# Optimization experiments

Hardware: AMD Instinct MI355X
Metric: run time of the kernel (lower is better)

## Reference

```python
import jax, jax.numpy as jnp
import numpy as np

N_NODES = 32000   # total nodes
NUM_GRAPHS = 32   # B
NODES_PER_GRAPH = 1000
N_EDGES = 256000
IN_DIM = 1024
HIDDEN = 256
C = 8             # clusters per graph


def sage_conv(x, src, dst, W_l, b_l, W_r, num_nodes):
    """PyG SAGEConv (mean aggr): out = lin_l(mean_{j in N(i)} x_j) + lin_r(x_i).
    lin_l has bias, lin_r does not. Zero in-degree -> zero aggregation."""
    msg = x[src]  # [E, F] gather from source nodes
    summed = jax.ops.segment_sum(msg, dst, num_segments=num_nodes)          # [N, F]
    cnt = jax.ops.segment_sum(jnp.ones(src.shape, x.dtype), dst, num_segments=num_nodes)  # [N]
    agg = jnp.where(cnt[:, None] > 0, summed / jnp.maximum(cnt, 1.0)[:, None], 0.0)
    return agg @ W_l + b_l + x @ W_r


def setup_inputs() -> dict:
    key = jax.random.key(0)
    ks = jax.random.split(key, 20)
    x = jax.random.normal(ks[0], (N_NODES, IN_DIM), dtype=jnp.float32)
    # edges strictly within each graph (nodes per graph contiguous)
    ge = jax.random.randint(ks[1], (N_EDGES,), 0, NUM_GRAPHS)
    sl = jax.random.randint(ks[2], (N_EDGES,), 0, NODES_PER_GRAPH)
    dl = jax.random.randint(ks[3], (N_EDGES,), 0, NODES_PER_GRAPH)
    edge_index = jnp.stack([ge * NODES_PER_GRAPH + sl, ge * NODES_PER_GRAPH + dl], axis=0)
    batch = jnp.arange(N_NODES, dtype=jnp.int32) // NODES_PER_GRAPH

    def lin(k, fi, fo):
        return jax.random.normal(k, (fi, fo), dtype=jnp.float32) / np.sqrt(fi)

    return {
        "x": x, "edge_index": edge_index, "batch": batch,
        # gnn_embed: SAGEConv(in_dim, hidden)
        "Wl1": lin(ks[4], IN_DIM, HIDDEN), "bl1": jnp.zeros((HIDDEN,), jnp.float32), "Wr1": lin(ks[5], IN_DIM, HIDDEN),
        # gnn_assign: SAGEConv(in_dim, C)
        "Wla": lin(ks[6], IN_DIM, C), "bla": jnp.zeros((C,), jnp.float32), "Wra": lin(ks[7], IN_DIM, C),
        # gnn_embed2: SAGEConv(hidden, hidden)
        "Wl2": lin(ks[8], HIDDEN, HIDDEN), "bl2": jnp.zeros((HIDDEN,), jnp.float32), "Wr2": lin(ks[9], HIDDEN, HIDDEN),
        # classifier MLP
        "Wc1": lin(ks[10], HIDDEN * C, HIDDEN), "bc1": jnp.zeros((HIDDEN,), jnp.float32),
        "Wc2": lin(ks[11], HIDDEN, 1), "bc2": jnp.zeros((1,), jnp.float32),
    }


def reference(x, edge_index, batch, Wl1, bl1, Wr1, Wla, bla, Wra, Wl2, bl2, Wr2, Wc1, bc1, Wc2, bc2):
    src, dst = edge_index[0], edge_index[1]
    n = x.shape[0]
    Z = jax.nn.relu(sage_conv(x, src, dst, Wl1, bl1, Wr1, n))   # [N, H]
    S = sage_conv(x, src, dst, Wla, bla, Wra, n)                 # [N, C]
    Ss = jax.nn.softmax(S, axis=-1)                              # row-softmax assignment
    # Per-graph DiffPool, batched via segment sums (replaces the python loop):
    # X_pool[g] = S_g^T Z_g
    Xp = jax.ops.segment_sum(Ss[:, :, None] * Z[:, None, :], batch, num_segments=NUM_GRAPHS)  # [B,C,H]
    # A_pool[g] = S_g^T A_g S_g  (A binary from to_dense_adj of within-graph edges)
    eg = batch[src]  # graph id per edge
    Ap = jax.ops.segment_sum(Ss[src][:, :, None] * Ss[dst][:, None, :], eg, num_segments=NUM_GRAPHS)  # [B,C,C]
    # dense_to_sparse(block_diag(A_pool)) drops edge weights -> binary block-diag adjacency.
    mask = (Ap != 0).astype(Z.dtype)   # edge i->j where A_pool[g,i,j] != 0
    deg = mask.sum(axis=1)             # in-degree of pooled node j: [B,C]
    agg = jnp.einsum('gij,gih->gjh', mask, Xp)  # mean over source pooled nodes
    agg = jnp.where(deg[:, :, None] > 0, agg / jnp.maximum(deg, 1.0)[:, :, None], 0.0)
    Zp = jax.nn.relu(agg @ Wl2 + bl2 + Xp @ Wr2)  # [B,C,H]
    g = Zp.reshape(NUM_GRAPHS, C * HIDDEN)
    h = jax.nn.relu(g @ Wc1 + bc1)
    return (h @ Wc2 + bc2).squeeze(-1)            # [B]
```

## Files before the change

kernel.cpp:

```cpp
#include <hip/hip_runtime.h>
#include <hip/hip_bf16.h>
#include <math.h>

#define N_NODES 32000
#define NUM_GRAPHS 32
#define NPG 1000
#define N_EDGES 256000
#define IN_DIM 1024
#define HID 256
#define NW 528
#define KBH 1040
#define WS_KS 33792
#define ZWORDS 139776

typedef _Float16 half8 __attribute__((ext_vector_type(8)));
typedef _Float16 half4 __attribute__((ext_vector_type(4)));
typedef float f32x4 __attribute__((ext_vector_type(4)));

__device__ __forceinline__ void gload16(const void* g, void* l) {
  __builtin_amdgcn_global_load_lds((const __attribute__((address_space(1))) void*)g,
                                   (__attribute__((address_space(3))) void*)l, 16, 0, 0);
}

__global__ __launch_bounds__(256) void prep_kernel(
    const float* __restrict__ Wl1, const float* __restrict__ Wr1,
    const float* __restrict__ Wla, const float* __restrict__ Wra,
    _Float16* __restrict__ WsT2, unsigned* __restrict__ zbuf)
{
  const int t = threadIdx.x;
  const int flat = blockIdx.y * 3 + blockIdx.x;
  for (int i = flat * 256 + t; i < ZWORDS; i += 384 * 256) zbuf[i] = 0u;

  const int kslot = blockIdx.y;
  const int n = blockIdx.x * 256 + t;
  if (n >= NW) return;
  const int k0 = kslot * 8;
  half8 o;
#pragma unroll
  for (int i = 0; i < 8; ++i) {
    const int k = k0 + i;
    float v;
    if (n < 256)      v = Wl1[(size_t)k * 256 + n];
    else if (n < 512) v = Wr1[(size_t)k * 256 + n - 256];
    else if (n < 520) v = Wla[(size_t)k * 8 + n - 512];
    else              v = Wra[(size_t)k * 8 + n - 520];
    o[i] = (_Float16)v;
  }
  const int ks = kslot >> 3, kb = kslot & 7;
  size_t off;
  if (n < 512) off = (size_t)ks * WS_KS + (size_t)(n >> 7) * 8192 + (kb * 128 + (n & 127)) * 8;
  else         off = (size_t)ks * WS_KS + 32768 + (kb * 16 + (n - 512)) * 8;
  *(half8*)&WsT2[off] = o;
}

__global__ __launch_bounds__(256) void xhalf(
    const float* __restrict__ x, _Float16* __restrict__ XH)
{
  const size_t i = ((size_t)blockIdx.x * 256 + threadIdx.x) * 8;
  float4 a = *(const float4*)(x + i);
  float4 b = *(const float4*)(x + i + 4);
  half8 h;
  h[0] = (_Float16)a.x; h[1] = (_Float16)a.y; h[2] = (_Float16)a.z; h[3] = (_Float16)a.w;
  h[4] = (_Float16)b.x; h[5] = (_Float16)b.y; h[6] = (_Float16)b.z; h[7] = (_Float16)b.w;
  *(half8*)&XH[i] = h;
}

__global__ __launch_bounds__(256) void gemm_mfma(
    const _Float16* __restrict__ XH, const _Float16* __restrict__ WsT2,
    _Float16* __restrict__ C)
{
  const int orig = blockIdx.x;
  const int xcd = orig & 7, idx = orig >> 3;
  const int g = (xcd < 2 ? xcd * 157 : 314 + (xcd - 2) * 156) + idx;
  const int pm = g / 5, nb = g % 5;
  const int m0 = pm * 128;

  __shared__ _Float16 AH[8 * KBH];
  __shared__ _Float16 Bs[8 * KBH];

  const int tid = threadIdx.x;
  const int w = tid >> 6, l = tid & 63;
  const int wr = w >> 1, wc = w & 1;
  const int r16 = l & 15, kb4 = l >> 4;

  int lpA[4];
  const _Float16* gA[4];
#pragma unroll
  for (int j = 0; j < 4; ++j) {
    const int c = tid + j * 256;
    const int kb = c >> 7, row = c & 127;
    lpA[j] = kb * KBH + row * 8;
    gA[j] = XH + (size_t)(m0 + row) * IN_DIM + kb * 8;
  }

  if (nb < 4) {
    const _Float16* gBbase = WsT2 + nb * 8192;

    f32x4 acc[4][4] = {};
    for (int ks = 0; ks < 16; ++ks) {
      const size_t ko = (size_t)ks * 64;
      const size_t bo = (size_t)ks * WS_KS;
      __syncthreads();
#pragma unroll
      for (int j = 0; j < 4; ++j) {
        gload16(gA[j] + ko, &AH[lpA[j]]);
        gload16(gBbase + bo + (tid + j * 256) * 8, &Bs[lpA[j]]);
      }
      __syncthreads();

#pragma unroll
      for (int s = 0; s < 2; ++s) {
        const int kblk = (s * 4 + kb4) * KBH;
        half8 bf[4];
#pragma unroll
        for (int n = 0; n < 4; ++n)
          bf[n] = *(half8*)&Bs[kblk + (wc * 64 + n * 16 + r16) * 8];
#pragma unroll
        for (int m = 0; m < 4; ++m) {
          half8 ah = *(half8*)&AH[kblk + (wr * 64 + m * 16 + r16) * 8];
#pragma unroll
          for (int n = 0; n < 4; ++n)
            acc[m][n] = __builtin_amdgcn_mfma_f32_16x16x32_f16(ah, bf[n], acc[m][n], 0, 0, 0);
        }
      }
    }
    const int crow0 = m0 + wr * 64 + ((l >> 4) << 2);
    const int ccol0 = nb * 128 + wc * 64 + r16;
#pragma unroll
    for (int m = 0; m < 4; ++m)
#pragma unroll
      for (int n = 0; n < 4; ++n)
#pragma unroll
        for (int r = 0; r < 4; ++r)
          C[(size_t)(crow0 + m * 16 + r) * NW + ccol0 + n * 16] = (_Float16)acc[m][n][r];
  } else {
    f32x4 acc2[2] = {};
    for (int ks = 0; ks < 16; ++ks) {
      const size_t ko = (size_t)ks * 64;
      const size_t bo = (size_t)ks * WS_KS + 32768;
      __syncthreads();
#pragma unroll
      for (int j = 0; j < 4; ++j) gload16(gA[j] + ko, &AH[lpA[j]]);
      if (tid < 128) gload16(WsT2 + bo + tid * 8, &Bs[tid * 8]);
      __syncthreads();

#pragma unroll
      for (int s = 0; s < 2; ++s) {
        const int kb = s * 4 + kb4;
        half8 bf = *(half8*)&Bs[(kb * 16 + r16) * 8];
#pragma unroll
        for (int m = 0; m < 2; ++m) {
          half8 ah = *(half8*)&AH[kb * KBH + (w * 32 + m * 16 + r16) * 8];
          acc2[m] = __builtin_amdgcn_mfma_f32_16x16x32_f16(ah, bf, acc2[m], 0, 0, 0);
        }
      }
    }
    const int crow0 = m0 + w * 32 + ((l >> 4) << 2);
    const int ccol0 = 512 + r16;
#pragma unroll
    for (int m = 0; m < 2; ++m)
#pragma unroll
      for (int r = 0; r < 4; ++r)
        C[(size_t)(crow0 + m * 16 + r) * NW + ccol0] = (_Float16)acc2[m][r];
  }
}

__global__ void count_deg(const int* __restrict__ dst, int* __restrict__ deg) {
  int e = blockIdx.x * blockDim.x + threadIdx.x;
  if (e < N_EDGES) atomicAdd(&deg[dst[e]], 1);
}

__global__ __launch_bounds__(1024) void scan_kernel(const int* __restrict__ deg,
                                                    int* __restrict__ offsets) {
  __shared__ int part[1024];
  const int t = threadIdx.x;
  const int base = t * 32;
  int vals[32];
  if (t < 1000) {
#pragma unroll
    for (int j = 0; j < 8; ++j) {
      int4 v = *(const int4*)(deg + base + j * 4);
      vals[j * 4 + 0] = v.x; vals[j * 4 + 1] = v.y;
      vals[j * 4 + 2] = v.z; vals[j * 4 + 3] = v.w;
    }
  } else {
#pragma unroll
    for (int i = 0; i < 32; ++i) vals[i] = 0;
  }
  int local[32];
  int s = 0;
#pragma unroll
  for (int i = 0; i < 32; ++i) { local[i] = s; s += vals[i]; }
  part[t] = s;
  __syncthreads();
  for (int off = 1; off < 1024; off <<= 1) {
    int v = (t >= off) ? part[t - off] : 0;
    __syncthreads();
    part[t] += v;
    __syncthreads();
  }
  int excl = part[t] - s;
  if (t < 1000) {
#pragma unroll
    for (int i = 0; i < 32; ++i) offsets[base + i] = excl + local[i];
  }
  if (t == 1023) offsets[N_NODES] = part[1023];
}

__global__ void scatter_kernel(const int* __restrict__ src, const int* __restrict__ dst,
                               const int* __restrict__ offsets, int* __restrict__ cursor,
                               int* __restrict__ srcSorted) {
  int e = blockIdx.x * blockDim.x + threadIdx.x;
  if (e < N_EDGES) {
    int d = dst[e];
    int pos = offsets[d] + atomicAdd(&cursor[d], 1);
    srcSorted[pos] = src[e];
  }
}

__global__ __launch_bounds__(256) void aggregate_node(
    const _Float16* __restrict__ C,
    const int* __restrict__ offsets, const int* __restrict__ srcSorted,
    const float* __restrict__ bl1, const float* __restrict__ bla,
    _Float16* __restrict__ Zh, float* __restrict__ Ss)
{
  const int bid = blockIdx.x;
  const int wv = threadIdx.x >> 6, lane = threadIdx.x & 63;
  const int node = (bid & 7) * 4000 + (bid >> 3) * 4 + wv;
  const int b = offsets[node], e = offsets[node + 1];
  const int cnt = e - b;
  const float4 blv = *(const float4*)(bl1 + 4 * lane);
  float a0 = 0.f, a1 = 0.f, a2 = 0.f, a3 = 0.f, sp = 0.f;
  int p = b;
  int sNext = (p < e) ? srcSorted[p] : 0;
  while (p < e) {
    const int s = sNext;
    ++p;
    sNext = (p < e) ? srcSorted[p] : 0;
    const _Float16* row = C + (size_t)s * NW;
    half4 v = *(const half4*)(row + 4 * lane);
    float spv = 0.f;
    if (lane < 8) spv = (float)row[512 + lane];
    a0 += (float)v[0]; a1 += (float)v[1]; a2 += (float)v[2]; a3 += (float)v[3];
    sp += spv;
  }
  const float inv = (cnt > 0) ? 1.f / (float)cnt : 0.f;
  const _Float16* self = C + (size_t)node * NW;
  half4 sv = *(const half4*)(self + 256 + 4 * lane);
  half4 zo;
  zo[0] = (_Float16)fmaxf(a0 * inv + blv.x + (float)sv[0], 0.f);
  zo[1] = (_Float16)fmaxf(a1 * inv + blv.y + (float)sv[1], 0.f);
  zo[2] = (_Float16)fmaxf(a2 * inv + blv.z + (float)sv[2], 0.f);
  zo[3] = (_Float16)fmaxf(a3 * inv + blv.w + (float)sv[3], 0.f);
  *(half4*)(Zh + (size_t)node * 256 + 4 * lane) = zo;

  float sval = 0.f;
  if (lane < 8) sval = sp * inv + bla[lane] + (float)self[520 + lane];
  float m = sval;
  m = fmaxf(m, __shfl_xor(m, 1));
  m = fmaxf(m, __shfl_xor(m, 2));
  m = fmaxf(m, __shfl_xor(m, 4));
  float ex = expf(sval - m);
  float su = ex;
  su += __shfl_xor(su, 1);
  su += __shfl_xor(su, 2);
  su += __shfl_xor(su, 4);
  if (lane < 8) Ss[(size_t)node * 8 + lane] = ex / su;
}

__global__ __launch_bounds__(256) void pool_kernel(
    const float* __restrict__ Ss, const _Float16* __restrict__ Zh,
    const int* __restrict__ offsets, const int* __restrict__ srcSorted,
    float* __restrict__ Xp, float* __restrict__ Ap)
{
  const int g = blockIdx.x >> 3;
  const int chunk = blockIdx.x & 7;
  const int n0 = g * NPG + chunk * 125;
  const int t = threadIdx.x;
  __shared__ float lSs[125][8];
  __shared__ float lAg[125][8];
  __shared__ float apTmp[4][64];

  if (t < 125) {
    const int node = n0 + t;
    float4 s0 = *(const float4*)&Ss[(size_t)node * 8];
    float4 s1 = *(const float4*)&Ss[(size_t)node * 8 + 4];
    lSs[t][0] = s0.x; lSs[t][1] = s0.y; lSs[t][2] = s0.z; lSs[t][3] = s0.w;
    lSs[t][4] = s1.x; lSs[t][5] = s1.y; lSs[t][6] = s1.z; lSs[t][7] = s1.w;
    float a[8] = {0.f, 0.f, 0.f, 0.f, 0.f, 0.f, 0.f, 0.f};
    const int b = offsets[node], e = offsets[node + 1];
    for (int p = b; p < e; ++p) {
      const int s = srcSorted[p];
      float4 v0 = *(const float4*)&Ss[(size_t)s * 8];
      float4 v1 = *(const float4*)&Ss[(size_t)s * 8 + 4];
      a[0] += v0.x; a[1] += v0.y; a[2] += v0.z; a[3] += v0.w;
      a[4] += v1.x; a[5] += v1.y; a[6] += v1.z; a[7] += v1.w;
    }
#pragma unroll
    for (int c = 0; c < 8; ++c) lAg[t][c] = a[c];
  }
  __syncthreads();
  {
    const int sl = t >> 6, i = (t >> 3) & 7, j = t & 7;
    float acc = 0.f;
    for (int n = sl; n < 125; n += 4) acc += lAg[n][i] * lSs[n][j];
    apTmp[sl][((i << 3) | j)] = acc;
  }
  __syncthreads();
  if (t < 64) atomicAdd(&Ap[g * 64 + t], apTmp[0][t] + apTmp[1][t] + apTmp[2][t] + apTmp[3][t]);
  float xc[8] = {0.f, 0.f, 0.f, 0.f, 0.f, 0.f, 0.f, 0.f};
  for (int n = 0; n < 125; ++n) {
    float zv = (float)Zh[(size_t)(n0 + n) * 256 + t];
#pragma unroll
    for (int c = 0; c < 8; ++c) xc[c] = fmaf(lSs[n][c], zv, xc[c]);
  }
#pragma unroll
  for (int c = 0; c < 8; ++c)
    atomicAdd(&Xp[((size_t)g * 8 + c) * 256 + t], xc[c]);
}

__global__ __launch_bounds__(256) void zpcls_kernel(
    const float* __restrict__ Xp, const float* __restrict__ Ap,
    const float* __restrict__ Wl2, const float* __restrict__ bl2,
    const float* __restrict__ Wr2, const float* __restrict__ Wc1,
    float* __restrict__ Hacc)
{
  const int g = blockIdx.x >> 3;
  const int j = blockIdx.x & 7;
  const int c = threadIdx.x;
  __shared__ float lXp[8][256];
  __shared__ float agg[256];
  __shared__ float zrow[256];
  __shared__ float lAp[64];
#pragma unroll
  for (int i = 0; i < 8; ++i) lXp[i][c] = Xp[((size_t)g * 8 + i) * 256 + c];
  if (c < 64) lAp[c] = Ap[g * 64 + c];
  __syncthreads();
  {
    float d = 0.f, s = 0.f;
#pragma unroll
    for (int i = 0; i < 8; ++i) {
      bool m = (lAp[i * 8 + j] != 0.f);
      d += m ? 1.f : 0.f;
      s += m ? lXp[i][c] : 0.f;
    }
    agg[c] = (d > 0.f) ? s / fmaxf(d, 1.f) : 0.f;
  }
  __syncthreads();
  float az = bl2[c];
#pragma unroll 8
  for (int k = 0; k < 256; ++k)
    az += agg[k] * Wl2[(size_t)k * 256 + c] + lXp[j][k] * Wr2[(size_t)k * 256 + c];
  zrow[c] = fmaxf(az, 0.f);
  __syncthreads();
  float h = 0.f;
  const float* wc1 = Wc1 + (size_t)(j * 256) * 256 + c;
#pragma unroll 8
  for (int k = 0; k < 256; ++k)
    h = fmaf(zrow[k], wc1[(size_t)k * 256], h);
  atomicAdd(&Hacc[g * 256 + c], h);
}

__global__ __launch_bounds__(256) void out_kernel(
    const float* __restrict__ Hacc, const float* __restrict__ bc1,
    const float* __restrict__ Wc2, const float* __restrict__ bc2,
    float* __restrict__ out)
{
  const int g = blockIdx.x;
  const int t = threadIdx.x;
  __shared__ float red[256];
  red[t] = fmaxf(Hacc[g * 256 + t] + bc1[t], 0.f) * Wc2[t];
  __syncthreads();
  for (int off = 128; off > 0; off >>= 1) {
    if (t < off) red[t] += red[t + off];
    __syncthreads();
  }
  if (t == 0) out[g] = red[0] + bc2[0];
}

extern "C" void kernel_launch(void* const* d_in, const int* in_sizes, int n_in,
                              void* d_out, int out_size, void* d_ws, size_t ws_size,
                              hipStream_t stream) {
  const float* x   = (const float*)d_in[0];
  const int*   ei  = (const int*)d_in[1];
  const float* Wl1 = (const float*)d_in[3];
  const float* bl1 = (const float*)d_in[4];
  const float* Wr1 = (const float*)d_in[5];
  const float* Wla = (const float*)d_in[6];
  const float* bla = (const float*)d_in[7];
  const float* Wra = (const float*)d_in[8];
  const float* Wl2 = (const float*)d_in[9];
  const float* bl2 = (const float*)d_in[10];
  const float* Wr2 = (const float*)d_in[11];
  const float* Wc1 = (const float*)d_in[12];
  const float* bc1 = (const float*)d_in[13];
  const float* Wc2 = (const float*)d_in[14];
  const float* bc2 = (const float*)d_in[15];
  float* out = (float*)d_out;

  _Float16* C    = (_Float16*)d_ws;
  _Float16* WsT2 = C + (size_t)32000 * NW;
  _Float16* XH   = WsT2 + 540672;
  _Float16* Zh   = XH + (size_t)32000 * 1024;
  float* Ss   = (float*)(Zh + (size_t)32000 * 256);
  float* Xp   = Ss + 256000;
  float* Ap   = Xp + 65536;
  int* deg     = (int*)(Ap + 2048);
  int* cursor  = deg + 32000;
  float* Hacc  = (float*)(cursor + 32000);
  int* offsets = (int*)(Hacc + 8192);
  int* srcS    = offsets + 32001;
  unsigned* zbuf = (unsigned*)Xp;

  const int* src = ei;
  const int* dst = ei + N_EDGES;

  prep_kernel<<<dim3(3, 128), 256, 0, stream>>>(Wl1, Wr1, Wla, Wra, WsT2, zbuf);
  xhalf<<<16000, 256, 0, stream>>>(x, XH);
  gemm_mfma<<<1250, 256, 0, stream>>>(XH, WsT2, C);
  count_deg<<<1000, 256, 0, stream>>>(dst, deg);
  scan_kernel<<<1, 1024, 0, stream>>>(deg, offsets);
  scatter_kernel<<<1000, 256, 0, stream>>>(src, dst, offsets, cursor, srcS);
  aggregate_node<<<8000, 256, 0, stream>>>(C, offsets, srcS, bl1, bla, Zh, Ss);
  pool_kernel<<<256, 256, 0, stream>>>(Ss, Zh, offsets, srcS, Xp, Ap);
  zpcls_kernel<<<256, 256, 0, stream>>>(Xp, Ap, Wl2, bl2, Wr2, Wc1, Hacc);
  out_kernel<<<32, 256, 0, stream>>>(Hacc, bc1, Wc2, bc2, out);
}
```

Before: 214.7 us.

## Load GEMM B operand directly to registers with prefetch; fuse degree count into xhalf

The GEMM no longer stages the weight operand through LDS. Weights are stored row-major as [n][k] in fp16, and each wave reads its B fragments straight from global memory into registers. It double-buffers them so the next k-step's loads are in flight while the current step computes, which is meant to cut LDS traffic and capacity. The separate degree-count kernel is folded into the fp32-to-fp16 conversion kernel, removing one launch. In exchange, B fragments are read redundantly across waves and blocks through cache, and the two register buffers raise register pressure.

```diff
diff --git a/kernel.cpp b/kernel.cpp
--- a/kernel.cpp
+++ b/kernel.cpp
@@ -10,7 +10,6 @@
 #define HID 256
 #define NW 528
 #define KBH 1040
-#define WS_KS 33792
 #define ZWORDS 139776
 
 typedef _Float16 half8 __attribute__((ext_vector_type(8)));
@@ -25,7 +24,7 @@
 __global__ __launch_bounds__(256) void prep_kernel(
     const float* __restrict__ Wl1, const float* __restrict__ Wr1,
     const float* __restrict__ Wla, const float* __restrict__ Wra,
-    _Float16* __restrict__ WsT2, unsigned* __restrict__ zbuf)
+    _Float16* __restrict__ WsT, unsigned* __restrict__ zbuf)
 {
   const int t = threadIdx.x;
   const int flat = blockIdx.y * 3 + blockIdx.x;
@@ -46,16 +45,16 @@
     else              v = Wra[(size_t)k * 8 + n - 520];
     o[i] = (_Float16)v;
   }
-  const int ks = kslot >> 3, kb = kslot & 7;
-  size_t off;
-  if (n < 512) off = (size_t)ks * WS_KS + (size_t)(n >> 7) * 8192 + (kb * 128 + (n & 127)) * 8;
-  else         off = (size_t)ks * WS_KS + 32768 + (kb * 16 + (n - 512)) * 8;
-  *(half8*)&WsT2[off] = o;
-}
-
-__global__ __launch_bounds__(256) void xhalf(
-    const float* __restrict__ x, _Float16* __restrict__ XH)
-{
+  *(half8*)&WsT[(size_t)n * IN_DIM + k0] = o;
+}
+
+__global__ __launch_bounds__(256) void xhalf_deg(
+    const float* __restrict__ x, _Float16* __restrict__ XH,
+    const int* __restrict__ dst, int* __restrict__ deg)
+{
+  const int e = blockIdx.x * 256 + threadIdx.x;
+  if (e < N_EDGES) atomicAdd(&deg[dst[e]], 1);
+
   const size_t i = ((size_t)blockIdx.x * 256 + threadIdx.x) * 8;
   float4 a = *(const float4*)(x + i);
   float4 b = *(const float4*)(x + i + 4);
@@ -66,7 +65,7 @@
 }
 
 __global__ __launch_bounds__(256) void gemm_mfma(
-    const _Float16* __restrict__ XH, const _Float16* __restrict__ WsT2,
+    const _Float16* __restrict__ XH, const _Float16* __restrict__ WsT,
     _Float16* __restrict__ C)
 {
   const int orig = blockIdx.x;
@@ -76,7 +75,6 @@
   const int m0 = pm * 128;
 
   __shared__ _Float16 AH[8 * KBH];
-  __shared__ _Float16 Bs[8 * KBH];
 
   const int tid = threadIdx.x;
   const int w = tid >> 6, l = tid & 63;
@@ -93,39 +91,63 @@
     gA[j] = XH + (size_t)(m0 + row) * IN_DIM + kb * 8;
   }
 
+#define STAGEA(KS)                                         \
+    do {                                                   \
+      const size_t ko_ = (size_t)(KS) * 64;                \
+      _Pragma("unroll")                                    \
+      for (int j_ = 0; j_ < 4; ++j_)                       \
+        gload16(gA[j_] + ko_, &AH[lpA[j_]]);               \
+    } while (0)
+
   if (nb < 4) {
-    const _Float16* gBbase = WsT2 + nb * 8192;
+    const int n0 = nb * 128;
+    const _Float16* pB = WsT + (size_t)(n0 + wc * 64 + r16) * IN_DIM + kb4 * 8;
+
+#define LOADB(KS, BF_)                                                              \
+    do {                                                                            \
+      const size_t ko_ = (size_t)(KS) * 64;                                         \
+      _Pragma("unroll")                                                             \
+      for (int s_ = 0; s_ < 2; ++s_)                                                \
+        _Pragma("unroll")                                                           \
+        for (int n_ = 0; n_ < 4; ++n_)                                              \
+          BF_[s_][n_] = *(const half8*)(pB + (size_t)n_ * 16 * IN_DIM + ko_ + s_ * 32); \
+    } while (0)
+
+#define COMPUTE(BF_)                                                                \
+    do {                                                                            \
+      _Pragma("unroll")                                                             \
+      for (int s_ = 0; s_ < 2; ++s_) {                                              \
+        const int kblk_ = (s_ * 4 + kb4) * KBH;                                     \
+        _Pragma("unroll")                                                           \
+        for (int m_ = 0; m_ < 4; ++m_) {                                            \
+          half8 ah_ = *(half8*)&AH[kblk_ + (wr * 64 + m_ * 16 + r16) * 8];          \
+          _Pragma("unroll")                                                         \
+          for (int n_ = 0; n_ < 4; ++n_)                                            \
+            acc[m_][n_] = __builtin_amdgcn_mfma_f32_16x16x32_f16(ah_, BF_[s_][n_], acc[m_][n_], 0, 0, 0); \
+        }                                                                           \
+      }                                                                             \
+    } while (0)
 
     f32x4 acc[4][4] = {};
-    for (int ks = 0; ks < 16; ++ks) {
-      const size_t ko = (size_t)ks * 64;
-      const size_t bo = (size_t)ks * WS_KS;
-      __syncthreads();
-#pragma unroll
-      for (int j = 0; j < 4; ++j) {
-        gload16(gA[j] + ko, &AH[lpA[j]]);
-        gload16(gBbase + bo + (tid + j * 256) * 8, &Bs[lpA[j]]);
-      }
-      __syncthreads();
-
-#pragma unroll
-      for (int s = 0; s < 2; ++s) {
-        const int kblk = (s * 4 + kb4) * KBH;
-        half8 bf[4];
-#pragma unroll
-        for (int n = 0; n < 4; ++n)
-          bf[n] = *(half8*)&Bs[kblk + (wc * 64 + n * 16 + r16) * 8];
-#pragma unroll
-        for (int m = 0; m < 4; ++m) {
-          half8 ah = *(half8*)&AH[kblk + (wr * 64 + m * 16 + r16) * 8];
-#pragma unroll
-          for (int n = 0; n < 4; ++n)
-            acc[m][n] = __builtin_amdgcn_mfma_f32_16x16x32_f16(ah, bf[n], acc[m][n], 0, 0, 0);
-        }
-      }
+    half8 bfA[2][4], bfB[2][4];
+    LOADB(0, bfA);
+    for (int ks2 = 0; ks2 < 16; ks2 += 2) {
+      __syncthreads();
+      STAGEA(ks2);
+      LOADB(ks2 + 1, bfB);
+      __syncthreads();
+      COMPUTE(bfA);
+      __syncthreads();
+      STAGEA(ks2 + 1);
+      if (ks2 + 2 < 16) LOADB(ks2 + 2, bfA);
+      __syncthreads();
+      COMPUTE(bfB);
     }
+#undef LOADB
+#undef COMPUTE
+
     const int crow0 = m0 + wr * 64 + ((l >> 4) << 2);
-    const int ccol0 = nb * 128 + wc * 64 + r16;
+    const int ccol0 = n0 + wc * 64 + r16;
 #pragma unroll
     for (int m = 0; m < 4; ++m)
 #pragma unroll
@@ -134,27 +156,46 @@
         for (int r = 0; r < 4; ++r)
           C[(size_t)(crow0 + m * 16 + r) * NW + ccol0 + n * 16] = (_Float16)acc[m][n][r];
   } else {
+    const _Float16* pB4 = WsT + (size_t)(512 + r16) * IN_DIM + kb4 * 8;
+
+#define LOADB4(KS, CF_)                                    \
+    do {                                                   \
+      const size_t ko_ = (size_t)(KS) * 64;                \
+      CF_[0] = *(const half8*)(pB4 + ko_);                 \
+      CF_[1] = *(const half8*)(pB4 + ko_ + 32);            \
+    } while (0)
+
+#define COMPUTE4(CF_)                                                               \
+    do {                                                                            \
+      _Pragma("unroll")                                                             \
+      for (int s_ = 0; s_ < 2; ++s_) {                                              \
+        const int kblk_ = (s_ * 4 + kb4) * KBH;                                     \
+        _Pragma("unroll")                                                           \
+        for (int m_ = 0; m_ < 2; ++m_) {                                            \
+          half8 ah_ = *(half8*)&AH[kblk_ + (w * 32 + m_ * 16 + r16) * 8];           \
+          acc2[m_] = __builtin_amdgcn_mfma_f32_16x16x32_f16(ah_, CF_[s_], acc2[m_], 0, 0, 0); \
+        }                                                                           \
+      }                                                                             \
+    } while (0)
+
     f32x4 acc2[2] = {};
-    for (int ks = 0; ks < 16; ++ks) {
-      const size_t ko = (size_t)ks * 64;
-      const size_t bo = (size_t)ks * WS_KS + 32768;
-      __syncthreads();
-#pragma unroll
-      for (int j = 0; j < 4; ++j) gload16(gA[j] + ko, &AH[lpA[j]]);
-      if (tid < 128) gload16(WsT2 + bo + tid * 8, &Bs[tid * 8]);
-      __syncthreads();
-
-#pragma unroll
-      for (int s = 0; s < 2; ++s) {
-        const int kb = s * 4 + kb4;
-        half8 bf = *(half8*)&Bs[(kb * 16 + r16) * 8];
-#pragma unroll
-        for (int m = 0; m < 2; ++m) {
-          half8 ah = *(half8*)&AH[kb * KBH + (w * 32 + m * 16 + r16) * 8];
-          acc2[m] = __builtin_amdgcn_mfma_f32_16x16x32_f16(ah, bf, acc2[m], 0, 0, 0);
-        }
-      }
+    half8 cfA[2], cfB[2];
+    LOADB4(0, cfA);
+    for (int ks2 = 0; ks2 < 16; ks2 += 2) {
+      __syncthreads();
+      STAGEA(ks2);
+      LOADB4(ks2 + 1, cfB);
+      __syncthreads();
+      COMPUTE4(cfA);
+      __syncthreads();
+      STAGEA(ks2 + 1);
+      if (ks2 + 2 < 16) LOADB4(ks2 + 2, cfA);
+      __syncthreads();
+      COMPUTE4(cfB);
     }
+#undef LOADB4
+#undef COMPUTE4
+
     const int crow0 = m0 + w * 32 + ((l >> 4) << 2);
     const int ccol0 = 512 + r16;
 #pragma unroll
@@ -163,11 +204,7 @@
       for (int r = 0; r < 4; ++r)
         C[(size_t)(crow0 + m * 16 + r) * NW + ccol0] = (_Float16)acc2[m][r];
   }
-}
-
-__global__ void count_deg(const int* __restrict__ dst, int* __restrict__ deg) {
-  int e = blockIdx.x * blockDim.x + threadIdx.x;
-  if (e < N_EDGES) atomicAdd(&deg[dst[e]], 1);
+#undef STAGEA
 }
 
 __global__ __launch_bounds__(1024) void scan_kernel(const int* __restrict__ deg,
@@ -399,8 +436,8 @@
   float* out = (float*)d_out;
 
   _Float16* C    = (_Float16*)d_ws;
-  _Float16* WsT2 = C + (size_t)32000 * NW;
-  _Float16* XH   = WsT2 + 540672;
+  _Float16* WsT  = C + (size_t)32000 * NW;
+  _Float16* XH   = WsT + 540672;
   _Float16* Zh   = XH + (size_t)32000 * 1024;
   float* Ss   = (float*)(Zh + (size_t)32000 * 256);
   float* Xp   = Ss + 256000;
@@ -415,10 +452,9 @@
   const int* src = ei;
   const int* dst = ei + N_EDGES;
 
-  prep_kernel<<<dim3(3, 128), 256, 0, stream>>>(Wl1, Wr1, Wla, Wra, WsT2, zbuf);
-  xhalf<<<16000, 256, 0, stream>>>(x, XH);
-  gemm_mfma<<<1250, 256, 0, stream>>>(XH, WsT2, C);
-  count_deg<<<1000, 256, 0, stream>>>(dst, deg);
+  prep_kernel<<<dim3(3, 128), 256, 0, stream>>>(Wl1, Wr1, Wla, Wra, WsT, zbuf);
+  xhalf_deg<<<16000, 256, 0, stream>>>(x, XH, dst, deg);
+  gemm_mfma<<<1250, 256, 0, stream>>>(XH, WsT, C);
   scan_kernel<<<1, 1024, 0, stream>>>(deg, offsets);
   scatter_kernel<<<1000, 256, 0, stream>>>(src, dst, offsets, cursor, srcS);
   aggregate_node<<<8000, 256, 0, stream>>>(C, offsets, srcS, bl1, bla, Zh, Ss);
```

Measured after the change: 282.8 us. 1.32x slower.
